# Kernel optimization log

Hardware: AMD Instinct MI355X
Metric: run time of the kernel (lower is better)

## Reference

```python
import jax, jax.numpy as jnp
import numpy as np

D_MODEL = 1024
D_PROJ = D_MODEL // 4


def setup_inputs() -> dict:
    key = jax.random.key(0)
    k1, k2, k3 = jax.random.split(key, 3)
    hidden_states = jax.random.normal(k1, (4, 2048, D_MODEL), dtype=jnp.float32)
    proj_w = jax.random.normal(k2, (D_PROJ, D_MODEL), dtype=jnp.float32) * 0.02
    proj_b = jnp.zeros((D_PROJ,), dtype=jnp.float32)
    clf_w = jax.random.normal(k3, (1, 1), dtype=jnp.float32) * 0.02
    clf_b = jnp.zeros((1,), dtype=jnp.float32)
    return {"hidden_states": hidden_states, "proj_w": proj_w, "proj_b": proj_b,
            "clf_w": clf_w, "clf_b": clf_b}


def reference(hidden_states, proj_w, proj_b, clf_w, clf_b):
    # h: [B, S, D/4]
    h = jax.nn.relu(jnp.einsum('bsd,pd->bsp', hidden_states, proj_w) + proj_b)
    # pairwise dot products == batched h @ h^T: [B, S, S]
    scores = jnp.einsum('bip,bjp->bij', h, h)
    # scalar affine classifier (Linear(1,1)) folded in
    return scores * clf_w[0, 0] + clf_b[0]
```

## Files before the change

kernel.cpp:

```cpp
#include <hip/hip_runtime.h>
#include <hip/hip_bf16.h>

typedef __bf16 bf16_t;
typedef __attribute__((ext_vector_type(8))) __bf16 bf16x8;
typedef __attribute__((ext_vector_type(4))) float f32x4;

#define SEQ    2048
#define DMODEL 1024
#define DPROJ  256
#define NBATCH 4

__device__ __forceinline__ bf16x8 cvt8(const float4& lo, const float4& hi) {
    bf16x8 v;
    v[0] = (bf16_t)lo.x; v[1] = (bf16_t)lo.y; v[2] = (bf16_t)lo.z; v[3] = (bf16_t)lo.w;
    v[4] = (bf16_t)hi.x; v[5] = (bf16_t)hi.y; v[6] = (bf16_t)hi.z; v[7] = (bf16_t)hi.w;
    return v;
}

__device__ __forceinline__ void gl_lds16(const void* g, void* l) {
    __builtin_amdgcn_global_load_lds(
        (const __attribute__((address_space(1))) unsigned int*)g,
        (__attribute__((address_space(3))) unsigned int*)l, 16, 0, 0);
}

__global__ __launch_bounds__(256) void proj_kernel(
    const float* __restrict__ X, const float* __restrict__ W,
    const float* __restrict__ bias, bf16_t* __restrict__ H)
{
    __shared__ __align__(16) bf16_t Xs[64 * 64];
    __shared__ __align__(16) bf16_t Ws[64 * 64];

    const int m0 = blockIdx.x * 64;
    const int n0 = blockIdx.y * 64;
    const int tid  = threadIdx.x;
    const int lane = tid & 63;
    const int wave = tid >> 6;
    const int quad = lane >> 4;
    const int l16  = lane & 15;
    const int wm = (wave & 1) * 32;
    const int wn = (wave >> 1) * 32;
    const int swz = l16 & 7;

    int srow[2], scol[2];
    bf16_t* lx[2];
    bf16_t* lw[2];
    #pragma unroll
    for (int r = 0; r < 2; ++r) {
        const int p = r * 256 + tid;
        srow[r] = p >> 3;
        scol[r] = p & 7;
        const int cs = (scol[r] ^ (srow[r] & 7)) * 8;
        lx[r] = Xs + srow[r] * 64 + cs;
        lw[r] = Ws + srow[r] * 64 + cs;
    }

    float4 xr[2][2], wr[2][2];
    #pragma unroll
    for (int r = 0; r < 2; ++r) {
        const float* gx = X + (size_t)(m0 + srow[r]) * DMODEL + scol[r] * 8;
        xr[r][0] = *(const float4*)gx;
        xr[r][1] = *(const float4*)(gx + 4);
        const float* gw = W + (size_t)(n0 + srow[r]) * DMODEL + scol[r] * 8;
        wr[r][0] = *(const float4*)gw;
        wr[r][1] = *(const float4*)(gw + 4);
    }

    f32x4 acc[2][2] = {};

    for (int kt = 0; kt < 16; ++kt) {
        __syncthreads();
        #pragma unroll
        for (int r = 0; r < 2; ++r) {
            *(bf16x8*)lx[r] = cvt8(xr[r][0], xr[r][1]);
            *(bf16x8*)lw[r] = cvt8(wr[r][0], wr[r][1]);
        }
        __syncthreads();

        if (kt < 15) {
            const int k0 = (kt + 1) * 64;
            #pragma unroll
            for (int r = 0; r < 2; ++r) {
                const float* gx = X + (size_t)(m0 + srow[r]) * DMODEL + k0 + scol[r] * 8;
                xr[r][0] = *(const float4*)gx;
                xr[r][1] = *(const float4*)(gx + 4);
                const float* gw = W + (size_t)(n0 + srow[r]) * DMODEL + k0 + scol[r] * 8;
                wr[r][0] = *(const float4*)gw;
                wr[r][1] = *(const float4*)(gw + 4);
            }
        }

        #pragma unroll
        for (int ks = 0; ks < 2; ++ks) {
            bf16x8 af[2], bfr[2];
            #pragma unroll
            for (int i = 0; i < 2; ++i) {
                const int ch = (((ks << 2) | quad) ^ swz) * 8;
                af[i]  = *(const bf16x8*)&Xs[(wm + i * 16 + l16) * 64 + ch];
                bfr[i] = *(const bf16x8*)&Ws[(wn + i * 16 + l16) * 64 + ch];
            }
            #pragma unroll
            for (int i = 0; i < 2; ++i)
                #pragma unroll
                for (int j = 0; j < 2; ++j)
                    acc[i][j] = __builtin_amdgcn_mfma_f32_16x16x32_bf16(
                        af[i], bfr[j], acc[i][j], 0, 0, 0);
        }
    }

    #pragma unroll
    for (int i = 0; i < 2; ++i) {
        #pragma unroll
        for (int j = 0; j < 2; ++j) {
            const int gn = n0 + wn + j * 16 + l16;
            const float bv = bias[gn];
            #pragma unroll
            for (int r = 0; r < 4; ++r) {
                const int gm = m0 + wm + i * 16 + quad * 4 + r;
                float v = acc[i][j][r] + bv;
                v = v > 0.f ? v : 0.f;
                H[(size_t)gm * DPROJ + gn] = (bf16_t)v;
            }
        }
    }
}

__global__ __launch_bounds__(512) void score_kernel(
    const bf16_t* __restrict__ H, const float* __restrict__ clf_w,
    const float* __restrict__ clf_b, float* __restrict__ Out)
{
    __shared__ __align__(16) bf16_t As[128 * 64];
    __shared__ __align__(16) bf16_t Bs[128 * 64];

    const int b  = blockIdx.z;
    const int m0 = blockIdx.x * 128;
    const int n0 = blockIdx.y * 128;
    const bf16_t* Hb = H + (size_t)b * SEQ * DPROJ;
    float* Ob = Out + (size_t)b * SEQ * SEQ;

    const int tid  = threadIdx.x;
    const int lane = tid & 63;
    const int wave = tid >> 6;
    const int quad = lane >> 4;
    const int l16  = lane & 15;
    const int wm = (wave & 3) * 32;
    const int wn = (wave >> 2) * 64;
    const int swz = l16 & 7;

    const bf16_t* gA[2];
    const bf16_t* gB[2];
    bf16_t* lA[2];
    bf16_t* lB[2];
    #pragma unroll
    for (int t = 0; t < 2; ++t) {
        const int g   = (wave * 2 + t) * 64 + lane;
        const int row = g >> 3;
        const int gc  = (g & 7) ^ (row & 7);
        gA[t] = Hb + (size_t)(m0 + row) * DPROJ + gc * 8;
        gB[t] = Hb + (size_t)(n0 + row) * DPROJ + gc * 8;
        lA[t] = As + (wave * 2 + t) * 512;
        lB[t] = Bs + (wave * 2 + t) * 512;
    }

    f32x4 acc[2][4] = {};

    for (int kt = 0; kt < 4; ++kt) {
        __syncthreads();
        #pragma unroll
        for (int t = 0; t < 2; ++t) {
            gl_lds16(gA[t], lA[t]);
            gl_lds16(gB[t], lB[t]);
        }
        __syncthreads();
        #pragma unroll
        for (int t = 0; t < 2; ++t) { gA[t] += 64; gB[t] += 64; }

        #pragma unroll
        for (int ks = 0; ks < 2; ++ks) {
            const int ch = (((ks << 2) | quad) ^ swz) * 8;
            bf16x8 af[2], bfr[4];
            #pragma unroll
            for (int i = 0; i < 2; ++i)
                af[i] = *(const bf16x8*)&As[(wm + i * 16 + l16) * 64 + ch];
            #pragma unroll
            for (int j = 0; j < 4; ++j)
                bfr[j] = *(const bf16x8*)&Bs[(wn + j * 16 + l16) * 64 + ch];
            #pragma unroll
            for (int i = 0; i < 2; ++i)
                #pragma unroll
                for (int j = 0; j < 4; ++j)
                    acc[i][j] = __builtin_amdgcn_mfma_f32_16x16x32_bf16(
                        af[i], bfr[j], acc[i][j], 0, 0, 0);
        }
    }

    const float scale = clf_w[0];
    const float off   = clf_b[0];
    #pragma unroll
    for (int i = 0; i < 2; ++i)
        #pragma unroll
        for (int j = 0; j < 4; ++j)
            #pragma unroll
            for (int r = 0; r < 4; ++r) {
                const int gm = m0 + wm + i * 16 + quad * 4 + r;
                const int gn = n0 + wn + j * 16 + l16;
                Ob[(size_t)gm * SEQ + gn] = acc[i][j][r] * scale + off;
            }
}

extern "C" void kernel_launch(void* const* d_in, const int* in_sizes, int n_in,
                              void* d_out, int out_size, void* d_ws, size_t ws_size,
                              hipStream_t stream) {
    const float* X    = (const float*)d_in[0];
    const float* W    = (const float*)d_in[1];
    const float* bias = (const float*)d_in[2];
    const float* clfw = (const float*)d_in[3];
    const float* clfb = (const float*)d_in[4];
    float* Out = (float*)d_out;
    bf16_t* H  = (bf16_t*)d_ws;

    dim3 g1(NBATCH * SEQ / 64, DPROJ / 64, 1);
    proj_kernel<<<g1, 256, 0, stream>>>(X, W, bias, H);

    dim3 g2(SEQ / 128, SEQ / 128, NBATCH);
    score_kernel<<<g2, 512, 0, stream>>>(H, clfw, clfb, Out);
}
```

Measured before the change: 131.0 us.

## Exploit symmetry of H·Hᵀ: compute upper-triangle tiles, mirror-write transpose; deepen proj prefetch

The score kernel now launches only upper-triangular tile pairs (bi<=bj) and writes each off-diagonal tile twice, once directly and once transposed with float4 stores, roughly halving MFMA and H-load work. The projection kernel switches to a two-stage register prefetch with a fully unrolled k-loop to hide global load latency. The output write volume is unchanged, so if the kernel is store-bandwidth bound the compute saving may matter less. The transposed stores have a different access pattern, and the extra prefetch registers raise register pressure in the projection kernel.

```diff
diff --git a/kernel.cpp b/kernel.cpp
--- a/kernel.cpp
+++ b/kernel.cpp
@@ -54,38 +54,45 @@
         lw[r] = Ws + srow[r] * 64 + cs;
     }
 
-    float4 xr[2][2], wr[2][2];
-    #pragma unroll
-    for (int r = 0; r < 2; ++r) {
-        const float* gx = X + (size_t)(m0 + srow[r]) * DMODEL + scol[r] * 8;
-        xr[r][0] = *(const float4*)gx;
-        xr[r][1] = *(const float4*)(gx + 4);
-        const float* gw = W + (size_t)(n0 + srow[r]) * DMODEL + scol[r] * 8;
-        wr[r][0] = *(const float4*)gw;
-        wr[r][1] = *(const float4*)(gw + 4);
+    float4 xr[2][2][2], wr[2][2][2];
+
+    #pragma unroll
+    for (int s = 0; s < 2; ++s) {
+        const int k0 = s * 64;
+        #pragma unroll
+        for (int r = 0; r < 2; ++r) {
+            const float* gx = X + (size_t)(m0 + srow[r]) * DMODEL + k0 + scol[r] * 8;
+            xr[s][r][0] = *(const float4*)gx;
+            xr[s][r][1] = *(const float4*)(gx + 4);
+            const float* gw = W + (size_t)(n0 + srow[r]) * DMODEL + k0 + scol[r] * 8;
+            wr[s][r][0] = *(const float4*)gw;
+            wr[s][r][1] = *(const float4*)(gw + 4);
+        }
     }
 
     f32x4 acc[2][2] = {};
 
+    #pragma unroll
     for (int kt = 0; kt < 16; ++kt) {
+        const int s = kt & 1;
         __syncthreads();
         #pragma unroll
         for (int r = 0; r < 2; ++r) {
-            *(bf16x8*)lx[r] = cvt8(xr[r][0], xr[r][1]);
-            *(bf16x8*)lw[r] = cvt8(wr[r][0], wr[r][1]);
-        }
-        __syncthreads();
-
-        if (kt < 15) {
-            const int k0 = (kt + 1) * 64;
+            *(bf16x8*)lx[r] = cvt8(xr[s][r][0], xr[s][r][1]);
+            *(bf16x8*)lw[r] = cvt8(wr[s][r][0], wr[s][r][1]);
+        }
+        __syncthreads();
+
+        if (kt < 14) {
+            const int k0 = (kt + 2) * 64;
             #pragma unroll
             for (int r = 0; r < 2; ++r) {
                 const float* gx = X + (size_t)(m0 + srow[r]) * DMODEL + k0 + scol[r] * 8;
-                xr[r][0] = *(const float4*)gx;
-                xr[r][1] = *(const float4*)(gx + 4);
+                xr[s][r][0] = *(const float4*)gx;
+                xr[s][r][1] = *(const float4*)(gx + 4);
                 const float* gw = W + (size_t)(n0 + srow[r]) * DMODEL + k0 + scol[r] * 8;
-                wr[r][0] = *(const float4*)gw;
-                wr[r][1] = *(const float4*)(gw + 4);
+                wr[s][r][0] = *(const float4*)gw;
+                wr[s][r][1] = *(const float4*)(gw + 4);
             }
         }
 
@@ -131,9 +138,12 @@
     __shared__ __align__(16) bf16_t As[128 * 64];
     __shared__ __align__(16) bf16_t Bs[128 * 64];
 
-    const int b  = blockIdx.z;
-    const int m0 = blockIdx.x * 128;
-    const int n0 = blockIdx.y * 128;
+    int t = blockIdx.x, bi = 0, rl = SEQ / 128;
+    while (t >= rl) { t -= rl; --rl; ++bi; }
+    const int bj = bi + t;
+    const int b  = blockIdx.y;
+    const int m0 = bi * 128;
+    const int n0 = bj * 128;
     const bf16_t* Hb = H + (size_t)b * SEQ * DPROJ;
     float* Ob = Out + (size_t)b * SEQ * SEQ;
 
@@ -151,14 +161,14 @@
     bf16_t* lA[2];
     bf16_t* lB[2];
     #pragma unroll
-    for (int t = 0; t < 2; ++t) {
-        const int g   = (wave * 2 + t) * 64 + lane;
+    for (int t2 = 0; t2 < 2; ++t2) {
+        const int g   = (wave * 2 + t2) * 64 + lane;
         const int row = g >> 3;
         const int gc  = (g & 7) ^ (row & 7);
-        gA[t] = Hb + (size_t)(m0 + row) * DPROJ + gc * 8;
-        gB[t] = Hb + (size_t)(n0 + row) * DPROJ + gc * 8;
-        lA[t] = As + (wave * 2 + t) * 512;
-        lB[t] = Bs + (wave * 2 + t) * 512;
+        gA[t2] = Hb + (size_t)(m0 + row) * DPROJ + gc * 8;
+        gB[t2] = Hb + (size_t)(n0 + row) * DPROJ + gc * 8;
+        lA[t2] = As + (wave * 2 + t2) * 512;
+        lB[t2] = Bs + (wave * 2 + t2) * 512;
     }
 
     f32x4 acc[2][4] = {};
@@ -166,13 +176,13 @@
     for (int kt = 0; kt < 4; ++kt) {
         __syncthreads();
         #pragma unroll
-        for (int t = 0; t < 2; ++t) {
-            gl_lds16(gA[t], lA[t]);
-            gl_lds16(gB[t], lB[t]);
-        }
-        __syncthreads();
-        #pragma unroll
-        for (int t = 0; t < 2; ++t) { gA[t] += 64; gB[t] += 64; }
+        for (int t2 = 0; t2 < 2; ++t2) {
+            gl_lds16(gA[t2], lA[t2]);
+            gl_lds16(gB[t2], lB[t2]);
+        }
+        __syncthreads();
+        #pragma unroll
+        for (int t2 = 0; t2 < 2; ++t2) { gA[t2] += 64; gB[t2] += 64; }
 
         #pragma unroll
         for (int ks = 0; ks < 2; ++ks) {
@@ -195,6 +205,7 @@
 
     const float scale = clf_w[0];
     const float off   = clf_b[0];
+
     #pragma unroll
     for (int i = 0; i < 2; ++i)
         #pragma unroll
@@ -205,6 +216,22 @@
                 const int gn = n0 + wn + j * 16 + l16;
                 Ob[(size_t)gm * SEQ + gn] = acc[i][j][r] * scale + off;
             }
+
+    if (bi != bj) {
+        #pragma unroll
+        for (int i = 0; i < 2; ++i)
+            #pragma unroll
+            for (int j = 0; j < 4; ++j) {
+                const int gn = n0 + wn + j * 16 + l16;
+                const int gm = m0 + wm + i * 16 + quad * 4;
+                float4 v;
+                v.x = acc[i][j][0] * scale + off;
+                v.y = acc[i][j][1] * scale + off;
+                v.z = acc[i][j][2] * scale + off;
+                v.w = acc[i][j][3] * scale + off;
+                *(float4*)&Ob[(size_t)gn * SEQ + gm] = v;
+            }
+    }
 }
 
 extern "C" void kernel_launch(void* const* d_in, const int* in_sizes, int n_in,
@@ -221,6 +248,7 @@
     dim3 g1(NBATCH * SEQ / 64, DPROJ / 64, 1);
     proj_kernel<<<g1, 256, 0, stream>>>(X, W, bias, H);
 
-    dim3 g2(SEQ / 128, SEQ / 128, NBATCH);
+    const int ntile = SEQ / 128;
+    dim3 g2(ntile * (ntile + 1) / 2, NBATCH);
     score_kernel<<<g2, 512, 0, stream>>>(H, clfw, clfb, Out);
 }
```

New measurement: 123.7 us. -5.5%, faster.
